# Performance work log

Measured on AMD Instinct MI355X. Metric: run time of the kernel, lower is better.

Reference implementation:

```python
import jax, jax.numpy as jnp
import numpy as np

B, C, H, W = 2, 256, 64, 64
N_HEAD = 4
GROUPS = 32
EPS = 1e-5


def setup_inputs() -> dict:
    key = jax.random.key(0)
    ks = jax.random.split(key, 6)
    x = jax.random.normal(ks[0], (B, C, H, W), dtype=jnp.float32)
    # GroupNorm affine (perturbed from torch default 1/0 so grads are nontrivial)
    gn_scale = 1.0 + 0.02 * jax.random.normal(ks[1], (C,), dtype=jnp.float32)
    gn_bias = 0.02 * jax.random.normal(ks[2], (C,), dtype=jnp.float32)
    # 1x1 convs == pointwise matmuls: qkv (bias=False), out (bias=True)
    w_qkv = 0.02 * jax.random.normal(ks[3], (3 * C, C), dtype=jnp.float32)
    w_out = 0.02 * jax.random.normal(ks[4], (C, C), dtype=jnp.float32)
    b_out = 0.02 * jax.random.normal(ks[5], (C,), dtype=jnp.float32)
    return {"x": x, "gn_scale": gn_scale, "gn_bias": gn_bias,
            "w_qkv": w_qkv, "w_out": w_out, "b_out": b_out}


def _group_norm(x, scale, bias):
    b, c, h, w = x.shape
    xr = x.reshape(b, GROUPS, c // GROUPS, h, w)
    mean = jnp.mean(xr, axis=(2, 3, 4), keepdims=True)
    var = jnp.var(xr, axis=(2, 3, 4), keepdims=True)
    xr = (xr - mean) * jax.lax.rsqrt(var + EPS)
    x = xr.reshape(b, c, h, w)
    return x * scale[None, :, None, None] + bias[None, :, None, None]


def reference(x, gn_scale, gn_bias, w_qkv, w_out, b_out):
    b, c, h, w = x.shape
    head_dim = c // N_HEAD
    n = h * w
    norm = _group_norm(x, gn_scale, gn_bias)
    # 1x1 conv -> pointwise channel matmul; flatten spatial to n = h*w tokens
    qkv = jnp.einsum('oc,bcn->bon', w_qkv, norm.reshape(b, c, n))
    qkv = qkv.reshape(b, N_HEAD, 3 * head_dim, n)
    q, k, v = jnp.split(qkv, 3, axis=2)  # each [b, n_head, head_dim, n]
    # NOTE: original scales by sqrt(channel), not sqrt(head_dim)
    attn = jnp.einsum('bndq,bndk->bnqk', q, k) / jnp.sqrt(jnp.float32(c))
    attn = jax.nn.softmax(attn, axis=-1)  # [b, n_head, n, n]
    out = jnp.einsum('bnqk,bndk->bndq', attn, v)  # [b, n_head, head_dim, n]
    out = out.reshape(b, c, n)
    out = jnp.einsum('oc,bcn->bon', w_out, out) + b_out[None, :, None]
    return out.reshape(b, c, h, w) + x
```

## Files before the change

### kernel.cpp

```cpp
#include <hip/hip_runtime.h>
#include <hip/hip_bf16.h>

#define Bz 2
#define Cc 256
#define Nn 4096
#define NH 4
#define HD 64
#define NG 32
#define CPG 8
#define EPSv 1e-5f
#define NSPLIT 4
#define GNPART 4

typedef __bf16 bf16x8 __attribute__((ext_vector_type(8)));
typedef __bf16 bf16x4 __attribute__((ext_vector_type(4)));
typedef float f32x4 __attribute__((ext_vector_type(4)));
using bf16_t = __hip_bfloat16;

#define MFMA(a, b, c) __builtin_amdgcn_mfma_f32_16x16x32_bf16(a, b, c, 0, 0, 0)

#define GLOAD_LDS(g, l)                                                        \
  __builtin_amdgcn_global_load_lds(                                            \
      (const __attribute__((address_space(1))) void*)(g),                      \
      (__attribute__((address_space(3))) void*)(l), 16, 0, 0)

#define EXP2(x)                                                                \
  ({ float _r, _x = (x); asm("v_exp_f32 %0, %1" : "=v"(_r) : "v"(_x)); _r; })

__device__ __forceinline__ bf16x8 ldb8(const bf16_t* p) {
  return *reinterpret_cast<const bf16x8*>(p);
}

__global__ __launch_bounds__(256) void gn_reduce(const float* __restrict__ x,
                                                 float* __restrict__ stats4) {
  int bg = blockIdx.x;
  int part = blockIdx.y;
  const float4* p4 = reinterpret_cast<const float4*>(
      x + (size_t)bg * (CPG * Nn) + (size_t)part * (CPG * Nn / GNPART));
  float s = 0.f, ss = 0.f;
  for (int i = threadIdx.x; i < CPG * Nn / GNPART / 4; i += 256) {
    float4 v = p4[i];
    s += v.x + v.y + v.z + v.w;
    ss += v.x * v.x + v.y * v.y + v.z * v.z + v.w * v.w;
  }
#pragma unroll
  for (int off = 32; off > 0; off >>= 1) {
    s += __shfl_down(s, off);
    ss += __shfl_down(ss, off);
  }
  __shared__ float ps[4], pss[4];
  int wid = threadIdx.x >> 6;
  if ((threadIdx.x & 63) == 0) { ps[wid] = s; pss[wid] = ss; }
  __syncthreads();
  if (threadIdx.x == 0) {
    stats4[(bg * GNPART + part) * 2] = ps[0] + ps[1] + ps[2] + ps[3];
    stats4[(bg * GNPART + part) * 2 + 1] = pss[0] + pss[1] + pss[2] + pss[3];
  }
}

__global__ __launch_bounds__(256) void gn_apply(const float* __restrict__ x,
    const float* __restrict__ stats4, const float* __restrict__ sc,
    const float* __restrict__ bi, bf16_t* __restrict__ normt) {
  int b = blockIdx.z, c0 = blockIdx.y * 64, n0 = blockIdx.x * 64;
  __shared__ __align__(16) __bf16 t[64][72];
  int cx = threadIdx.x & 15, cy0 = threadIdx.x >> 4;
  const float inv = 1.f / (float)(CPG * Nn);
#pragma unroll
  for (int j = 0; j < 4; j++) {
    int c = c0 + cy0 + j * 16;
    int bg = b * NG + (c >> 3);
    float S = stats4[bg * 8] + stats4[bg * 8 + 2] + stats4[bg * 8 + 4] + stats4[bg * 8 + 6];
    float SS = stats4[bg * 8 + 1] + stats4[bg * 8 + 3] + stats4[bg * 8 + 5] + stats4[bg * 8 + 7];
    float mean = S * inv;
    float rstd = rsqrtf(SS * inv - mean * mean + EPSv);
    float a = rstd * sc[c];
    float bb = bi[c] - mean * a;
    float4 v = *reinterpret_cast<const float4*>(x + ((size_t)b * Cc + c) * Nn + n0 + cx * 4);
    bf16x4 w;
    w[0] = (__bf16)(v.x * a + bb); w[1] = (__bf16)(v.y * a + bb);
    w[2] = (__bf16)(v.z * a + bb); w[3] = (__bf16)(v.w * a + bb);
    *reinterpret_cast<bf16x4*>(&t[cy0 + j * 16][cx * 4]) = w;
  }
  __syncthreads();
  int ny = threadIdx.x >> 2, ch0 = threadIdx.x & 3;
#pragma unroll
  for (int j = 0; j < 2; j++) {
    int ch = ch0 + j * 4;
    bf16x8 o;
#pragma unroll
    for (int jj = 0; jj < 8; jj++) o[jj] = t[ch * 8 + jj][ny];
    *reinterpret_cast<bf16x8*>(normt + ((size_t)b * Nn + n0 + ny) * Cc + c0 + ch * 8) = o;
  }
}

__global__ __launch_bounds__(256) void conv_w(const float* __restrict__ wq,
    const float* __restrict__ wo, bf16_t* __restrict__ wqb,
    bf16_t* __restrict__ wob) {
  int i = blockIdx.x * 256 + threadIdx.x;
  if (i < 768 * Cc) wqb[i] = __float2bfloat16(wq[i]);
  if (i < Cc * Cc) wob[i] = __float2bfloat16(wo[i]);
}

__global__ __launch_bounds__(512) void qkv_gemm(const bf16_t* __restrict__ normt,
    const bf16_t* __restrict__ w, bf16_t* __restrict__ Qt,
    bf16_t* __restrict__ Kt, bf16_t* __restrict__ V) {
  int b = blockIdx.z;
  int o0 = blockIdx.y * 64;
  int n0 = blockIdx.x * 128;
  int tid = threadIdx.x;
  int wid = tid >> 6, lane = tid & 63;
  int lr = lane & 15, lk = lane >> 4;

  __shared__ __align__(16) char smem[64 * 256 * 2];
  bf16_t* wbuf = (bf16_t*)smem;
  __bf16* t = (__bf16*)smem;

#pragma unroll
  for (int rnd = 0; rnd < 4; rnd++) {
    int u = rnd * 512 + tid;
    int row = u >> 5, cu = u & 31;
    int cus = (cu & 24) | ((cu & 7) ^ (row & 7));
    GLOAD_LDS(w + (size_t)(o0 + row) * Cc + cus * 8, &wbuf[u * 8]);
  }
  const bf16_t* an = normt + ((size_t)b * Nn + n0 + wid * 16 + lr) * Cc + lk * 8;
  f32x4 acc[4] = {};
  __syncthreads();
#pragma unroll
  for (int kk = 0; kk < Cc / 32; kk++) {
    bf16x8 a = ldb8(an + kk * 32);
#pragma unroll
    for (int os = 0; os < 4; os++) {
      bf16x8 bb = ldb8(&wbuf[(os * 16 + lr) * Cc + (((kk * 4 + lk) ^ (lr & 7)) * 8)]);
      acc[os] = MFMA(a, bb, acc[os]);
    }
  }
  __syncthreads();
#pragma unroll
  for (int os = 0; os < 4; os++)
#pragma unroll
    for (int r = 0; r < 4; r++)
      t[(wid * 16 + lk * 4 + r) * 80 + os * 16 + lr] = (__bf16)acc[os][r];
  __syncthreads();
  int h = o0 / 192;
  int part = (o0 % 192) / 64;
  if (part < 2) {
    bf16_t* dst = (part == 0 ? Qt : Kt) + (size_t)(b * NH + h) * Nn * HD + (size_t)n0 * HD;
    int n = tid >> 2, dch = (tid & 3) * 16;
    bf16x8 o1 = ldb8(reinterpret_cast<const bf16_t*>(&t[n * 80 + dch]));
    bf16x8 o2 = ldb8(reinterpret_cast<const bf16_t*>(&t[n * 80 + dch + 8]));
    *reinterpret_cast<bf16x8*>(dst + (size_t)n * HD + dch) = o1;
    *reinterpret_cast<bf16x8*>(dst + (size_t)n * HD + dch + 8) = o2;
  } else {
    bf16_t* dst = V + (size_t)(b * NH + h) * HD * Nn + n0;
    int d = tid >> 3, nch = (tid & 7) * 16;
    bf16x8 o1, o2;
#pragma unroll
    for (int j = 0; j < 8; j++) {
      o1[j] = t[(nch + j) * 80 + d];
      o2[j] = t[(nch + 8 + j) * 80 + d];
    }
    *reinterpret_cast<bf16x8*>(dst + (size_t)d * Nn + nch) = o1;
    *reinterpret_cast<bf16x8*>(dst + (size_t)d * Nn + nch + 8) = o2;
  }
}

__global__ __launch_bounds__(512, 4) void attn_kern(const bf16_t* __restrict__ Qt,
    const bf16_t* __restrict__ Kt, const bf16_t* __restrict__ V,
    bf16_t* __restrict__ Opart, float* __restrict__ ml) {
  int z = blockIdx.z;
  int b = z & 1, sp = z >> 1;
  int h = blockIdx.y;
  int wid = threadIdx.x >> 6, lane = threadIdx.x & 63;
  int lr = lane & 15, lk = lane >> 4;
  int q0 = blockIdx.x * 128 + wid * 16;
  size_t bh = (size_t)(b * NH + h);
  const bf16_t* qp = Qt + (bh * Nn + q0 + lr) * HD + lk * 8;
  bf16x8 aq0 = ldb8(qp), aq1 = ldb8(qp + 32);
  const bf16_t* kglob = Kt + bh * Nn * HD;
  const bf16_t* vglob = V + bh * HD * Nn;
  int kbeg = sp * (Nn / NSPLIT);

  __shared__ __align__(16) bf16_t kbuf[2][64 * 64];
  __shared__ __align__(16) bf16_t vbuf[2][64 * 64];
  __shared__ __align__(16) bf16_t plds[8][16 * 72];
  bf16_t* myp = plds[wid];

  int su = (wid & 3) * 64 + lane;
  int srow = su >> 3, sc = su & 7;
  int swz = (sc ^ (srow & 7)) * 8;
  const bf16_t* ksrc = kglob + (size_t)(kbeg + srow) * HD + swz;
  const bf16_t* vsrc = vglob + (size_t)srow * Nn + kbeg + swz;

  f32x4 acc[4] = {};
  float m_r = -1e30f, l_r = 0.f;
  const float lam = 0.0625f * 1.44269504088896f;
  const int NT = (Nn / NSPLIT) / 64;

#define STAGE(buf, t)                                                          \
  do {                                                                         \
    if (wid < 4) {                                                             \
      GLOAD_LDS(ksrc + (size_t)(t) * 64 * HD, &kbuf[buf][(wid & 3) * 512]);    \
      GLOAD_LDS(ksrc + (size_t)(t) * 64 * HD + 32 * HD,                        \
                &kbuf[buf][2048 + (wid & 3) * 512]);                           \
    } else {                                                                   \
      GLOAD_LDS(vsrc + (size_t)(t) * 64, &vbuf[buf][(wid & 3) * 512]);         \
      GLOAD_LDS(vsrc + (size_t)(t) * 64 + (size_t)32 * Nn,                     \
                &vbuf[buf][2048 + (wid & 3) * 512]);                           \
    }                                                                          \
  } while (0)

#define FADDR(m, kk) ((16 * (m) + lr) * 64 + (((4 * (kk) + lk) ^ (lr & 7)) * 8))

#define STEP(t, buf)                                                           \
  do {                                                                         \
    __syncthreads();                                                           \
    STAGE(buf ^ 1, (t) + 1);                                                   \
    const bf16_t* kb = kbuf[buf];                                              \
    const bf16_t* vb = vbuf[buf];                                              \
    f32x4 s0 = {}, s1 = {}, s2 = {}, s3 = {};                                  \
    __builtin_amdgcn_s_setprio(1);                                             \
    s0 = MFMA(ldb8(kb + FADDR(0, 0)), aq0, s0);                                \
    s0 = MFMA(ldb8(kb + FADDR(0, 1)), aq1, s0);                                \
    s1 = MFMA(ldb8(kb + FADDR(1, 0)), aq0, s1);                                \
    s1 = MFMA(ldb8(kb + FADDR(1, 1)), aq1, s1);                                \
    s2 = MFMA(ldb8(kb + FADDR(2, 0)), aq0, s2);                                \
    s2 = MFMA(ldb8(kb + FADDR(2, 1)), aq1, s2);                                \
    s3 = MFMA(ldb8(kb + FADDR(3, 0)), aq0, s3);                                \
    s3 = MFMA(ldb8(kb + FADDR(3, 1)), aq1, s3);                                \
    __builtin_amdgcn_s_setprio(0);                                             \
    float pm = fmaxf(fmaxf(fmaxf(s0[0], s0[1]), fmaxf(s0[2], s0[3])),          \
                     fmaxf(fmaxf(s1[0], s1[1]), fmaxf(s1[2], s1[3])));         \
    pm = fmaxf(pm, fmaxf(fmaxf(fmaxf(s2[0], s2[1]), fmaxf(s2[2], s2[3])),      \
                         fmaxf(fmaxf(s3[0], s3[1]), fmaxf(s3[2], s3[3]))));    \
    if (!__all(pm <= m_r + 64.f)) {       \
      float pw = fmaxf(pm, __shfl_xor(pm, 16));                                \
      pw = fmaxf(pw, __shfl_xor(pw, 32));                                      \
      float mn = fmaxf(m_r, pw);                                               \
      float sf = EXP2((m_r - mn) * lam);                                       \
      m_r = mn;                                                                \
      l_r *= sf;                                                               \
      acc[0] = acc[0] * sf; acc[1] = acc[1] * sf;                              \
      acc[2] = acc[2] * sf; acc[3] = acc[3] * sf;                              \
    }                                                                          \
    float mnl = m_r * lam;                                                     \
    f32x4 p0, p1, p2, p3;                                                      \
    _Pragma("unroll") for (int r = 0; r < 4; r++) {                            \
      p0[r] = EXP2(s0[r] * lam - mnl);                                         \
      p1[r] = EXP2(s1[r] * lam - mnl);                                         \
      p2[r] = EXP2(s2[r] * lam - mnl);                                         \
      p3[r] = EXP2(s3[r] * lam - mnl);                                         \
    }                                                                          \
    f32x4 ps = (p0 + p1) + (p2 + p3);                                          \
    l_r += (ps[0] + ps[1]) + (ps[2] + ps[3]);                                  \
    bf16x4 w0, w1, w2, w3;                                                     \
    _Pragma("unroll") for (int r = 0; r < 4; r++) {                            \
      w0[r] = (__bf16)p0[r]; w1[r] = (__bf16)p1[r];                            \
      w2[r] = (__bf16)p2[r]; w3[r] = (__bf16)p3[r];                            \
    }                                                                          \
    *reinterpret_cast<bf16x4*>(myp + lr * 72 + lk * 4) = w0;                   \
    *reinterpret_cast<bf16x4*>(myp + lr * 72 + 16 + lk * 4) = w1;              \
    *reinterpret_cast<bf16x4*>(myp + lr * 72 + 32 + lk * 4) = w2;              \
    *reinterpret_cast<bf16x4*>(myp + lr * 72 + 48 + lk * 4) = w3;              \
    bf16x8 pa0 = ldb8(myp + lr * 72 + lk * 8);                                 \
    bf16x8 pa1 = ldb8(myp + lr * 72 + 32 + lk * 8);                            \
    __builtin_amdgcn_s_setprio(1);                                             \
    acc[0] = MFMA(ldb8(vb + FADDR(0, 0)), pa0, acc[0]);                        \
    acc[0] = MFMA(ldb8(vb + FADDR(0, 1)), pa1, acc[0]);                        \
    acc[1] = MFMA(ldb8(vb + FADDR(1, 0)), pa0, acc[1]);                        \
    acc[1] = MFMA(ldb8(vb + FADDR(1, 1)), pa1, acc[1]);                        \
    acc[2] = MFMA(ldb8(vb + FADDR(2, 0)), pa0, acc[2]);                        \
    acc[2] = MFMA(ldb8(vb + FADDR(2, 1)), pa1, acc[2]);                        \
    acc[3] = MFMA(ldb8(vb + FADDR(3, 0)), pa0, acc[3]);                        \
    acc[3] = MFMA(ldb8(vb + FADDR(3, 1)), pa1, acc[3]);                        \
    __builtin_amdgcn_s_setprio(0);                                             \
  } while (0)

  STAGE(0, 0);
  for (int t = 0; t < NT; t += 2) {
    STEP(t, 0);
    STEP(t + 1, 1);
  }
#undef STEP
#undef STAGE
#undef FADDR

  l_r += __shfl_xor(l_r, 16);
  l_r += __shfl_xor(l_r, 32);
  float inv_l = 1.f / l_r;
  bf16_t* obase = Opart + (((size_t)z * NH + h) * Nn + q0 + lr) * HD + lk * 4;
#pragma unroll
  for (int dt = 0; dt < 4; dt++) {
    bf16x4 ov;
#pragma unroll
    for (int r = 0; r < 4; r++) ov[r] = (__bf16)(acc[dt][r] * inv_l);
    *reinterpret_cast<bf16x4*>(obase + dt * 16) = ov;
  }
  if (lk == 0) {
    float2 mlv = make_float2(m_r, l_r);
    *reinterpret_cast<float2*>(ml + (((size_t)z * NH + h) * Nn + q0 + lr) * 2) = mlv;
  }
}

__global__ __launch_bounds__(256) void attn_merge(const bf16_t* __restrict__ Opart,
    const float* __restrict__ ml, bf16_t* __restrict__ At) {
  int gid = blockIdx.x * 256 + threadIdx.x;
  int d0 = (gid & 7) * 8;
  int q = (gid >> 3) & (Nn - 1);
  int h = (gid >> 15) & (NH - 1);
  int b = gid >> 17;
  const float lam = 0.0625f * 1.44269504088896f;
  size_t zi[NSPLIT];
  float mv[NSPLIT], lv[NSPLIT], wv[NSPLIT];
  float M = -1e30f;
#pragma unroll
  for (int s = 0; s < NSPLIT; s++) {
    zi[s] = ((size_t)(s * Bz + b) * NH + h) * Nn + q;
    mv[s] = ml[zi[s] * 2];
    lv[s] = ml[zi[s] * 2 + 1];
    M = fmaxf(M, mv[s]);
  }
  float L = 0.f;
#pragma unroll
  for (int s = 0; s < NSPLIT; s++) {
    wv[s] = lv[s] * EXP2((mv[s] - M) * lam);
    L += wv[s];
  }
  float invL = 1.f / L;
  float o[8] = {};
#pragma unroll
  for (int s = 0; s < NSPLIT; s++) {
    bf16x8 a = ldb8(Opart + zi[s] * HD + d0);
#pragma unroll
    for (int r = 0; r < 8; r++) o[r] += (float)a[r] * wv[s];
  }
  bf16x8 ov;
#pragma unroll
  for (int r = 0; r < 8; r++) ov[r] = (__bf16)(o[r] * invL);
  *reinterpret_cast<bf16x8*>(At + ((size_t)b * Nn + q) * Cc + h * HD + d0) = ov;
}

__global__ __launch_bounds__(256) void out_gemm(const bf16_t* __restrict__ At,
    const bf16_t* __restrict__ w, const float* __restrict__ bo,
    const float* __restrict__ x, float* __restrict__ out) {
  int b = blockIdx.z;
  int o0 = blockIdx.y * 64;
  int n0 = blockIdx.x * 64;
  int tid = threadIdx.x;
  int wid = tid >> 6;
  int lane = tid & 63;
  int lr = lane & 15, lk = lane >> 4;

  __shared__ __align__(16) char smem[64 * 256 * 2];
  bf16_t* wbuf = (bf16_t*)smem;
  float(*t)[68] = (float(*)[68])smem;

#pragma unroll
  for (int rnd = 0; rnd < 8; rnd++) {
    int u = rnd * 256 + tid;
    int row = u >> 5, cu = u & 31;
    int cus = (cu & 24) | ((cu & 7) ^ (row & 7));
    GLOAD_LDS(w + (size_t)(o0 + row) * Cc + cus * 8, &wbuf[u * 8]);
  }
  const bf16_t* aa = At + ((size_t)b * Nn + n0 + wid * 16 + lr) * Cc + lk * 8;
  f32x4 acc[4] = {};
  __syncthreads();
#pragma unroll
  for (int kk = 0; kk < Cc / 32; kk++) {
    bf16x8 a = ldb8(aa + kk * 32);
#pragma unroll
    for (int os = 0; os < 4; os++) {
      bf16x8 bb = ldb8(&wbuf[(os * 16 + lr) * Cc + (((kk * 4 + lk) ^ (lr & 7)) * 8)]);
      acc[os] = MFMA(a, bb, acc[os]);
    }
  }
  __syncthreads();
#pragma unroll
  for (int os = 0; os < 4; os++)
#pragma unroll
    for (int r = 0; r < 4; r++)
      t[wid * 16 + lk * 4 + r][os * 16 + lr] = acc[os][r];
  __syncthreads();
  int orow = tid >> 2;
  int nch = (tid & 3) * 16;
  size_t base = ((size_t)b * Cc + o0 + orow) * Nn + n0 + nch;
  float bv = bo[o0 + orow];
#pragma unroll
  for (int j = 0; j < 16; j++)
    out[base + j] = t[nch + j][orow] + bv + x[base + j];
}

extern "C" void kernel_launch(void* const* d_in, const int* in_sizes, int n_in,
                              void* d_out, int out_size, void* d_ws, size_t ws_size,
                              hipStream_t stream) {
  const float* x = (const float*)d_in[0];
  const float* gn_scale = (const float*)d_in[1];
  const float* gn_bias = (const float*)d_in[2];
  const float* w_qkv = (const float*)d_in[3];
  const float* w_out = (const float*)d_in[4];
  const float* b_out = (const float*)d_in[5];
  float* out = (float*)d_out;
  char* ws = (char*)d_ws;

  float* stats4 = (float*)(ws + 0);
  bf16_t* wout_b = (bf16_t*)(ws + 4096);
  bf16_t* Qt = (bf16_t*)(ws + 139264);
  bf16_t* At = (bf16_t*)(ws + 139264);
  bf16_t* Kt = (bf16_t*)(ws + 4333568);
  bf16_t* V = (bf16_t*)(ws + 8527872);
  bf16_t* wqkv_b = (bf16_t*)(ws + 12722176);
  bf16_t* normt = (bf16_t*)(ws + 13115392);
  bf16_t* Opart = (bf16_t*)(ws + 12722176);
  float* ml = (float*)(ws + 29499392);

  conv_w<<<768, 256, 0, stream>>>(w_qkv, w_out, wqkv_b, wout_b);
  gn_reduce<<<dim3(Bz * NG, GNPART), 256, 0, stream>>>(x, stats4);
  gn_apply<<<dim3(Nn / 64, Cc / 64, Bz), 256, 0, stream>>>(x, stats4, gn_scale, gn_bias, normt);
  qkv_gemm<<<dim3(Nn / 128, 12, Bz), 512, 0, stream>>>(normt, wqkv_b, Qt, Kt, V);
  attn_kern<<<dim3(Nn / 128, NH, Bz * NSPLIT), 512, 0, stream>>>(Qt, Kt, V, Opart, ml);
  attn_merge<<<Bz * NH * Nn * HD / 8 / 256, 256, 0, stream>>>(Opart, ml, At);
  out_gemm<<<dim3(Nn / 64, Cc / 64, Bz), 256, 0, stream>>>(At, wout_b, b_out, x, out);
}
```

Before: 90.73 us.

## Fuse Q/K/V parts per block in qkv_gemm and streamline attention inner loop

qkv_gemm now computes all three 64-row output parts (Q, K, V) of one head in a single block. It loads the normalized activation fragments into registers once and reuses them across the three weight tiles, which cuts the grid from 12 to 4 blocks in y and removes repeated global reads of normt. The attention kernel switches to one flat LDS buffer addressed by precomputed byte offsets. It uses v_max3_f32 for the row-max reduction and accumulates the softmax denominator as a vector, reducing it only at the end. The qkv change trades parallelism (fewer blocks) and serialized weight reloads with extra barriers for less activation traffic.

```diff
diff --git a/kernel.cpp b/kernel.cpp
--- a/kernel.cpp
+++ b/kernel.cpp
@@ -26,6 +26,10 @@
 
 #define EXP2(x)                                                                \
   ({ float _r, _x = (x); asm("v_exp_f32 %0, %1" : "=v"(_r) : "v"(_x)); _r; })
+
+#define MAX3F(a, b, c)                                                         \
+  ({ float _m; asm("v_max3_f32 %0, %1, %2, %3"                                 \
+                   : "=v"(_m) : "v"(a), "v"(b), "v"(c)); _m; })
 
 __device__ __forceinline__ bf16x8 ldb8(const bf16_t* p) {
   return *reinterpret_cast<const bf16x8*>(p);
@@ -105,62 +109,64 @@
     const bf16_t* __restrict__ w, bf16_t* __restrict__ Qt,
     bf16_t* __restrict__ Kt, bf16_t* __restrict__ V) {
   int b = blockIdx.z;
-  int o0 = blockIdx.y * 64;
+  int h = blockIdx.y;
   int n0 = blockIdx.x * 128;
   int tid = threadIdx.x;
   int wid = tid >> 6, lane = tid & 63;
   int lr = lane & 15, lk = lane >> 4;
 
-  __shared__ __align__(16) char smem[64 * 256 * 2];
-  bf16_t* wbuf = (bf16_t*)smem;
-  __bf16* t = (__bf16*)smem;
-
-#pragma unroll
-  for (int rnd = 0; rnd < 4; rnd++) {
-    int u = rnd * 512 + tid;
-    int row = u >> 5, cu = u & 31;
-    int cus = (cu & 24) | ((cu & 7) ^ (row & 7));
-    GLOAD_LDS(w + (size_t)(o0 + row) * Cc + cus * 8, &wbuf[u * 8]);
-  }
+  __shared__ __align__(16) bf16_t wbuf[64 * 256];
+  __shared__ __align__(16) __bf16 tt[128 * 80];
+
   const bf16_t* an = normt + ((size_t)b * Nn + n0 + wid * 16 + lr) * Cc + lk * 8;
-  f32x4 acc[4] = {};
-  __syncthreads();
-#pragma unroll
-  for (int kk = 0; kk < Cc / 32; kk++) {
-    bf16x8 a = ldb8(an + kk * 32);
-#pragma unroll
-    for (int os = 0; os < 4; os++) {
-      bf16x8 bb = ldb8(&wbuf[(os * 16 + lr) * Cc + (((kk * 4 + lk) ^ (lr & 7)) * 8)]);
-      acc[os] = MFMA(a, bb, acc[os]);
+  bf16x8 a[8];
+#pragma unroll
+  for (int kk = 0; kk < 8; kk++) a[kk] = ldb8(an + kk * 32);
+
+#pragma unroll
+  for (int part = 0; part < 3; part++) {
+    int o0 = h * 192 + part * 64;
+#pragma unroll
+    for (int rnd = 0; rnd < 4; rnd++) {
+      int u = rnd * 512 + tid;
+      int row = u >> 5, cu = u & 31;
+      int cus = (cu & 24) | ((cu & 7) ^ (row & 7));
+      GLOAD_LDS(w + (size_t)(o0 + row) * Cc + cus * 8, &wbuf[u * 8]);
     }
-  }
-  __syncthreads();
-#pragma unroll
-  for (int os = 0; os < 4; os++)
-#pragma unroll
-    for (int r = 0; r < 4; r++)
-      t[(wid * 16 + lk * 4 + r) * 80 + os * 16 + lr] = (__bf16)acc[os][r];
-  __syncthreads();
-  int h = o0 / 192;
-  int part = (o0 % 192) / 64;
-  if (part < 2) {
-    bf16_t* dst = (part == 0 ? Qt : Kt) + (size_t)(b * NH + h) * Nn * HD + (size_t)n0 * HD;
-    int n = tid >> 2, dch = (tid & 3) * 16;
-    bf16x8 o1 = ldb8(reinterpret_cast<const bf16_t*>(&t[n * 80 + dch]));
-    bf16x8 o2 = ldb8(reinterpret_cast<const bf16_t*>(&t[n * 80 + dch + 8]));
-    *reinterpret_cast<bf16x8*>(dst + (size_t)n * HD + dch) = o1;
-    *reinterpret_cast<bf16x8*>(dst + (size_t)n * HD + dch + 8) = o2;
-  } else {
-    bf16_t* dst = V + (size_t)(b * NH + h) * HD * Nn + n0;
-    int d = tid >> 3, nch = (tid & 7) * 16;
-    bf16x8 o1, o2;
-#pragma unroll
-    for (int j = 0; j < 8; j++) {
-      o1[j] = t[(nch + j) * 80 + d];
-      o2[j] = t[(nch + 8 + j) * 80 + d];
+    __syncthreads();
+    f32x4 acc[4] = {};
+#pragma unroll
+    for (int kk = 0; kk < 8; kk++)
+#pragma unroll
+      for (int os = 0; os < 4; os++) {
+        bf16x8 bb = ldb8(&wbuf[(os * 16 + lr) * Cc + (((kk * 4 + lk) ^ (lr & 7)) * 8)]);
+        acc[os] = MFMA(a[kk], bb, acc[os]);
+      }
+#pragma unroll
+    for (int os = 0; os < 4; os++)
+#pragma unroll
+      for (int r = 0; r < 4; r++)
+        tt[(wid * 16 + lk * 4 + r) * 80 + os * 16 + lr] = (__bf16)acc[os][r];
+    __syncthreads();
+    if (part < 2) {
+      bf16_t* dst = (part == 0 ? Qt : Kt) + (size_t)(b * NH + h) * Nn * HD + (size_t)n0 * HD;
+      int n = tid >> 2, dch = (tid & 3) * 16;
+      bf16x8 o1 = ldb8(reinterpret_cast<const bf16_t*>(&tt[n * 80 + dch]));
+      bf16x8 o2 = ldb8(reinterpret_cast<const bf16_t*>(&tt[n * 80 + dch + 8]));
+      *reinterpret_cast<bf16x8*>(dst + (size_t)n * HD + dch) = o1;
+      *reinterpret_cast<bf16x8*>(dst + (size_t)n * HD + dch + 8) = o2;
+    } else {
+      bf16_t* dst = V + (size_t)(b * NH + h) * HD * Nn + n0;
+      int d = tid >> 3, nch = (tid & 7) * 16;
+      bf16x8 o1, o2;
+#pragma unroll
+      for (int j = 0; j < 8; j++) {
+        o1[j] = tt[(nch + j) * 80 + d];
+        o2[j] = tt[(nch + 8 + j) * 80 + d];
+      }
+      *reinterpret_cast<bf16x8*>(dst + (size_t)d * Nn + nch) = o1;
+      *reinterpret_cast<bf16x8*>(dst + (size_t)d * Nn + nch + 8) = o2;
     }
-    *reinterpret_cast<bf16x8*>(dst + (size_t)d * Nn + nch) = o1;
-    *reinterpret_cast<bf16x8*>(dst + (size_t)d * Nn + nch + 8) = o2;
   }
 }
 
@@ -180,65 +186,71 @@
   const bf16_t* vglob = V + bh * HD * Nn;
   int kbeg = sp * (Nn / NSPLIT);
 
-  __shared__ __align__(16) bf16_t kbuf[2][64 * 64];
-  __shared__ __align__(16) bf16_t vbuf[2][64 * 64];
-  __shared__ __align__(16) bf16_t plds[8][16 * 72];
-  bf16_t* myp = plds[wid];
+  __shared__ __align__(16) char lds[51200];
 
   int su = (wid & 3) * 64 + lane;
-  int srow = su >> 3, sc = su & 7;
-  int swz = (sc ^ (srow & 7)) * 8;
+  int srow = su >> 3, scc = su & 7;
+  int swz = (scc ^ (srow & 7)) * 8;
   const bf16_t* ksrc = kglob + (size_t)(kbeg + srow) * HD + swz;
   const bf16_t* vsrc = vglob + (size_t)srow * Nn + kbeg + swz;
 
+  int x0 = lr & 7;
+  int aK = lr * 128 + ((lk ^ x0) * 16);
+  int aK1 = aK ^ 64;
+  int pwo = 32768 + wid * 2304 + lr * 144 + lk * 8;
+  int pro = 32768 + wid * 2304 + lr * 144 + lk * 16;
+
   f32x4 acc[4] = {};
-  float m_r = -1e30f, l_r = 0.f;
+  f32x4 lacc = {};
+  float m_r = -1e30f;
   const float lam = 0.0625f * 1.44269504088896f;
   const int NT = (Nn / NSPLIT) / 64;
+
+#define LD8(off) (*reinterpret_cast<const bf16x8*>(lds + (off)))
 
 #define STAGE(buf, t)                                                          \
   do {                                                                         \
     if (wid < 4) {                                                             \
-      GLOAD_LDS(ksrc + (size_t)(t) * 64 * HD, &kbuf[buf][(wid & 3) * 512]);    \
+      GLOAD_LDS(ksrc + (size_t)(t) * 64 * HD,                                  \
+                lds + (buf) * 8192 + (wid & 3) * 1024);                        \
       GLOAD_LDS(ksrc + (size_t)(t) * 64 * HD + 32 * HD,                        \
-                &kbuf[buf][2048 + (wid & 3) * 512]);                           \
+                lds + (buf) * 8192 + (wid & 3) * 1024 + 4096);                 \
     } else {                                                                   \
-      GLOAD_LDS(vsrc + (size_t)(t) * 64, &vbuf[buf][(wid & 3) * 512]);         \
+      GLOAD_LDS(vsrc + (size_t)(t) * 64,                                       \
+                lds + 16384 + (buf) * 8192 + (wid & 3) * 1024);                \
       GLOAD_LDS(vsrc + (size_t)(t) * 64 + (size_t)32 * Nn,                     \
-                &vbuf[buf][2048 + (wid & 3) * 512]);                           \
+                lds + 16384 + (buf) * 8192 + (wid & 3) * 1024 + 4096);         \
     }                                                                          \
   } while (0)
-
-#define FADDR(m, kk) ((16 * (m) + lr) * 64 + (((4 * (kk) + lk) ^ (lr & 7)) * 8))
 
 #define STEP(t, buf)                                                           \
   do {                                                                         \
     __syncthreads();                                                           \
     STAGE(buf ^ 1, (t) + 1);                                                   \
-    const bf16_t* kb = kbuf[buf];                                              \
-    const bf16_t* vb = vbuf[buf];                                              \
     f32x4 s0 = {}, s1 = {}, s2 = {}, s3 = {};                                  \
     __builtin_amdgcn_s_setprio(1);                                             \
-    s0 = MFMA(ldb8(kb + FADDR(0, 0)), aq0, s0);                                \
-    s0 = MFMA(ldb8(kb + FADDR(0, 1)), aq1, s0);                                \
-    s1 = MFMA(ldb8(kb + FADDR(1, 0)), aq0, s1);                                \
-    s1 = MFMA(ldb8(kb + FADDR(1, 1)), aq1, s1);                                \
-    s2 = MFMA(ldb8(kb + FADDR(2, 0)), aq0, s2);                                \
-    s2 = MFMA(ldb8(kb + FADDR(2, 1)), aq1, s2);                                \
-    s3 = MFMA(ldb8(kb + FADDR(3, 0)), aq0, s3);                                \
-    s3 = MFMA(ldb8(kb + FADDR(3, 1)), aq1, s3);                                \
+    s0 = MFMA(LD8(aK + (buf) * 8192), aq0, s0);                                \
+    s0 = MFMA(LD8(aK1 + (buf) * 8192), aq1, s0);                               \
+    s1 = MFMA(LD8(aK + (buf) * 8192 + 2048), aq0, s1);                         \
+    s1 = MFMA(LD8(aK1 + (buf) * 8192 + 2048), aq1, s1);                        \
+    s2 = MFMA(LD8(aK + (buf) * 8192 + 4096), aq0, s2);                         \
+    s2 = MFMA(LD8(aK1 + (buf) * 8192 + 4096), aq1, s2);                        \
+    s3 = MFMA(LD8(aK + (buf) * 8192 + 6144), aq0, s3);                         \
+    s3 = MFMA(LD8(aK1 + (buf) * 8192 + 6144), aq1, s3);                        \
     __builtin_amdgcn_s_setprio(0);                                             \
-    float pm = fmaxf(fmaxf(fmaxf(s0[0], s0[1]), fmaxf(s0[2], s0[3])),          \
-                     fmaxf(fmaxf(s1[0], s1[1]), fmaxf(s1[2], s1[3])));         \
-    pm = fmaxf(pm, fmaxf(fmaxf(fmaxf(s2[0], s2[1]), fmaxf(s2[2], s2[3])),      \
-                         fmaxf(fmaxf(s3[0], s3[1]), fmaxf(s3[2], s3[3]))));    \
-    if (!__all(pm <= m_r + 64.f)) {       \
-      float pw = fmaxf(pm, __shfl_xor(pm, 16));                                \
-      pw = fmaxf(pw, __shfl_xor(pw, 32));                                      \
-      float mn = fmaxf(m_r, pw);                                               \
+    float _t0 = MAX3F(s0[0], s0[1], s0[2]);                                    \
+    float _t1 = MAX3F(s0[3], s1[0], s1[1]);                                    \
+    float _t2 = MAX3F(s1[2], s1[3], s2[0]);                                    \
+    float _t3 = MAX3F(s2[1], s2[2], s2[3]);                                    \
+    float _t4 = MAX3F(s3[0], s3[1], s3[2]);                                    \
+    float pm = fmaxf(MAX3F(_t0, _t1, _t2), MAX3F(_t3, _t4, s3[3]));            \
+    if (!__all(pm <= m_r + 64.f)) {      \
+      float pmw = fmaxf(pm, __shfl_xor(pm, 16));                               \
+      pmw = fmaxf(pmw, __shfl_xor(pmw, 32));                                   \
+      float mn = fmaxf(m_r, pmw);                                              \
       float sf = EXP2((m_r - mn) * lam);                                       \
       m_r = mn;                                                                \
-      l_r *= sf;                                                               \
+      lacc = lacc * sf;                                                        \
       acc[0] = acc[0] * sf; acc[1] = acc[1] * sf;                              \
       acc[2] = acc[2] * sf; acc[3] = acc[3] * sf;                              \
     }                                                                          \
@@ -250,28 +262,27 @@
       p2[r] = EXP2(s2[r] * lam - mnl);                                         \
       p3[r] = EXP2(s3[r] * lam - mnl);                                         \
     }                                                                          \
-    f32x4 ps = (p0 + p1) + (p2 + p3);                                          \
-    l_r += (ps[0] + ps[1]) + (ps[2] + ps[3]);                                  \
+    lacc += (p0 + p1) + (p2 + p3);                                             \
     bf16x4 w0, w1, w2, w3;                                                     \
     _Pragma("unroll") for (int r = 0; r < 4; r++) {                            \
       w0[r] = (__bf16)p0[r]; w1[r] = (__bf16)p1[r];                            \
       w2[r] = (__bf16)p2[r]; w3[r] = (__bf16)p3[r];                            \
     }                                                                          \
-    *reinterpret_cast<bf16x4*>(myp + lr * 72 + lk * 4) = w0;                   \
-    *reinterpret_cast<bf16x4*>(myp + lr * 72 + 16 + lk * 4) = w1;              \
-    *reinterpret_cast<bf16x4*>(myp + lr * 72 + 32 + lk * 4) = w2;              \
-    *reinterpret_cast<bf16x4*>(myp + lr * 72 + 48 + lk * 4) = w3;              \
-    bf16x8 pa0 = ldb8(myp + lr * 72 + lk * 8);                                 \
-    bf16x8 pa1 = ldb8(myp + lr * 72 + 32 + lk * 8);                            \
+    *reinterpret_cast<bf16x4*>(lds + pwo) = w0;                                \
+    *reinterpret_cast<bf16x4*>(lds + pwo + 32) = w1;                           \
+    *reinterpret_cast<bf16x4*>(lds + pwo + 64) = w2;                           \
+    *reinterpret_cast<bf16x4*>(lds + pwo + 96) = w3;                           \
+    bf16x8 pa0 = LD8(pro);                                                     \
+    bf16x8 pa1 = LD8(pro + 64);                                                \
     __builtin_amdgcn_s_setprio(1);                                             \
-    acc[0] = MFMA(ldb8(vb + FADDR(0, 0)), pa0, acc[0]);                        \
-    acc[0] = MFMA(ldb8(vb + FADDR(0, 1)), pa1, acc[0]);                        \
-    acc[1] = MFMA(ldb8(vb + FADDR(1, 0)), pa0, acc[1]);                        \
-    acc[1] = MFMA(ldb8(vb + FADDR(1, 1)), pa1, acc[1]);                        \
-    acc[2] = MFMA(ldb8(vb + FADDR(2, 0)), pa0, acc[2]);                        \
-    acc[2] = MFMA(ldb8(vb + FADDR(2, 1)), pa1, acc[2]);                        \
-    acc[3] = MFMA(ldb8(vb + FADDR(3, 0)), pa0, acc[3]);                        \
-    acc[3] = MFMA(ldb8(vb + FADDR(3, 1)), pa1, acc[3]);                        \
+    acc[0] = MFMA(LD8(aK + 16384 + (buf) * 8192), pa0, acc[0]);                \
+    acc[0] = MFMA(LD8(aK1 + 16384 + (buf) * 8192), pa1, acc[0]);               \
+    acc[1] = MFMA(LD8(aK + 16384 + (buf) * 8192 + 2048), pa0, acc[1]);         \
+    acc[1] = MFMA(LD8(aK1 + 16384 + (buf) * 8192 + 2048), pa1, acc[1]);        \
+    acc[2] = MFMA(LD8(aK + 16384 + (buf) * 8192 + 4096), pa0, acc[2]);         \
+    acc[2] = MFMA(LD8(aK1 + 16384 + (buf) * 8192 + 4096), pa1, acc[2]);        \
+    acc[3] = MFMA(LD8(aK + 16384 + (buf) * 8192 + 6144), pa0, acc[3]);         \
+    acc[3] = MFMA(LD8(aK1 + 16384 + (buf) * 8192 + 6144), pa1, acc[3]);        \
     __builtin_amdgcn_s_setprio(0);                                             \
   } while (0)
 
@@ -282,8 +293,9 @@
   }
 #undef STEP
 #undef STAGE
-#undef FADDR
-
+#undef LD8
+
+  float l_r = (lacc[0] + lacc[1]) + (lacc[2] + lacc[3]);
   l_r += __shfl_xor(l_r, 16);
   l_r += __shfl_xor(l_r, 32);
   float inv_l = 1.f / l_r;
@@ -415,7 +427,7 @@
   conv_w<<<768, 256, 0, stream>>>(w_qkv, w_out, wqkv_b, wout_b);
   gn_reduce<<<dim3(Bz * NG, GNPART), 256, 0, stream>>>(x, stats4);
   gn_apply<<<dim3(Nn / 64, Cc / 64, Bz), 256, 0, stream>>>(x, stats4, gn_scale, gn_bias, normt);
-  qkv_gemm<<<dim3(Nn / 128, 12, Bz), 512, 0, stream>>>(normt, wqkv_b, Qt, Kt, V);
+  qkv_gemm<<<dim3(Nn / 128, NH, Bz), 512, 0, stream>>>(normt, wqkv_b, Qt, Kt, V);
   attn_kern<<<dim3(Nn / 128, NH, Bz * NSPLIT), 512, 0, stream>>>(Qt, Kt, V, Opart, ml);
   attn_merge<<<Bz * NH * Nn * HD / 8 / 256, 256, 0, stream>>>(Opart, ml, At);
   out_gemm<<<dim3(Nn / 64, Cc / 64, Bz), 256, 0, stream>>>(At, wout_b, b_out, x, out);
```

Result: no change. 89.29 us (-1.6%).
